# Performance work log

Hardware: AMD Instinct MI355X
Metric: run time of the kernel (lower is better)

The kernel has to match this reference:

```python
import jax, jax.numpy as jnp
import numpy as np

B, N, L, OUT = 64, 100, 32, 3
EDGE_SIZES = [64, 64]   # edge MLP widths per mp step
NODE_SIZES = [64, 32]   # node MLP widths per mp step
ALPHA = 0.1             # leaky relu slope
NUM_MPS = 2
EPS = 1e-12             # for differentiable euclidean norm


def _lin_init(key, fan_in, fan_out):
    k1, k2 = jax.random.split(key)
    s = 1.0 / np.sqrt(fan_in)
    w = jax.random.uniform(k1, (fan_in, fan_out), jnp.float32, -s, s)
    b = jax.random.uniform(k2, (fan_out,), jnp.float32, -s, s)
    return w, b


def setup_inputs() -> dict:
    key = jax.random.key(0)
    ks = iter(jax.random.split(key, 32))
    inp = {"x": jax.random.normal(next(ks), (B, L), jnp.float32)}
    # global latent map: Linear(L, N*L)
    inp["lin_w"], inp["lin_b"] = _lin_init(next(ks), L, N * L)
    d = L
    for i in range(NUM_MPS):
        e_in = 2 * d + 1  # [x_i, x_j, dist_ij]
        inp[f"e{i}_w0"], inp[f"e{i}_b0"] = _lin_init(next(ks), e_in, EDGE_SIZES[0])
        inp[f"e{i}_w1"], inp[f"e{i}_b1"] = _lin_init(next(ks), EDGE_SIZES[0], EDGE_SIZES[1])
        n_in = d + EDGE_SIZES[1]  # [x, aggregated edges]
        inp[f"n{i}_w0"], inp[f"n{i}_b0"] = _lin_init(next(ks), n_in, NODE_SIZES[0])
        inp[f"n{i}_w1"], inp[f"n{i}_b1"] = _lin_init(next(ks), NODE_SIZES[0], NODE_SIZES[1])
        d = NODE_SIZES[1]
    inp["out_w"], inp["out_b"] = _lin_init(next(ks), d, OUT)
    return inp


def _mlp(h, layers, alpha):
    for w, b in layers:
        h = jax.nn.leaky_relu(h @ w + b, alpha)
    return h


def _forward(x, lin_w, lin_b,
             e0_w0, e0_b0, e0_w1, e0_b1, n0_w0, n0_b0, n0_w1, n0_b1,
             e1_w0, e1_b0, e1_w1, e1_b1, n1_w0, n1_b0, n1_w1, n1_b1,
             out_w, out_b):
    # latent map: [B, L] -> [B, N, L]
    h = (x @ lin_w + lin_b).reshape(-1, N, L)
    steps = [
        ([(e0_w0, e0_b0), (e0_w1, e0_b1)], [(n0_w0, n0_b0), (n0_w1, n0_b1)]),
        ([(e1_w0, e1_b0), (e1_w1, e1_b1)], [(n1_w0, n1_b0), (n1_w1, n1_b1)]),
    ]
    for edge_layers, node_layers in steps:
        b, n, d = h.shape
        xi = h[:, :, None, :]  # [B, N, 1, d] (receiver)
        xj = h[:, None, :, :]  # [B, 1, N, d] (sender)
        # euclidean pairwise distance, eps for differentiability at 0
        dist = jnp.sqrt(jnp.sum((xi - xj) ** 2, axis=-1, keepdims=True) + EPS)
        e_in = jnp.concatenate([
            jnp.broadcast_to(xi, (b, n, n, d)),
            jnp.broadcast_to(xj, (b, n, n, d)),
            dist,
        ], axis=-1)                       # [B, N, N, 2d+1]
        A = _mlp(e_in, edge_layers, ALPHA)  # [B, N, N, e_out]
        agg = A.sum(axis=2)               # sum over senders -> [B, N, e_out]
        h = _mlp(jnp.concatenate([h, agg], axis=-1), node_layers, ALPHA)
    out = h @ out_w + out_b               # [B, N, OUT]
    return jnp.tanh(out)                  # normalize_output=True


def reference(x, lin_w, lin_b,
              e0_w0, e0_b0, e0_w1, e0_b1, n0_w0, n0_b0, n0_w1, n0_b1,
              e1_w0, e1_b0, e1_w1, e1_b1, n1_w0, n1_b0, n1_w1, n1_b1,
              out_w, out_b):
    return _forward(x, lin_w, lin_b,
                    e0_w0, e0_b0, e0_w1, e0_b1, n0_w0, n0_b0, n0_w1, n0_b1,
                    e1_w0, e1_b0, e1_w1, e1_b1, n1_w0, n1_b0, n1_w1, n1_b1,
                    out_w, out_b)
```

## Files before the change

kernel.cpp:

```cpp
#include <hip/hip_runtime.h>

#define NB 64
#define NN 100
#define DL 32
#define BN (NB * NN)

typedef _Float16 f16x8 __attribute__((ext_vector_type(8)));
typedef _Float16 f16x4 __attribute__((ext_vector_type(4)));
typedef float f32x4 __attribute__((ext_vector_type(4)));

static __device__ __forceinline__ float lrelu(float x) { return fmaxf(x, 0.1f * x); }

__global__ __launch_bounds__(256) void k_pre(
    const float* __restrict__ x, const float* __restrict__ lw, const float* __restrict__ lb,
    const float* __restrict__ ew0, const float* __restrict__ eb0,
    const float* __restrict__ w1a, const float* __restrict__ w1b,
    float* __restrict__ h, float* __restrict__ U, float* __restrict__ V,
    _Float16* __restrict__ PW) {
    int blk = blockIdx.x;
    int t = threadIdx.x;
    if (blk >= 1600) {
        int step = blk - 1600;
        const float* w1 = step ? w1b : w1a;
        _Float16* dst = PW + step * 4096;
#pragma unroll
        for (int u = 0; u < 16; ++u) {
            int idx = t * 16 + u;
            int jj = idx & 7, lane = (idx >> 3) & 63, hf = (idx >> 9) & 1, kt = idx >> 10;
            int c = hf * 32 + (lane >> 4) * 8 + jj;
            int k = kt * 16 + (lane & 15);
            dst[idx] = (_Float16)w1[c * 64 + k];
        }
        return;
    }
    __shared__ float xs[DL];
    __shared__ float hs[4][DL];
    int row0 = blk * 4;
    int b = row0 / NN;
    if (t < DL) xs[t] = x[b * DL + t];
    __syncthreads();
    if (t < 128) {
        int ni = t >> 5, c = t & 31;
        int n = (row0 + ni) % NN;
        float s = lb[n * DL + c];
#pragma unroll
        for (int cc = 0; cc < DL; ++cc) s += xs[cc] * lw[cc * 3200 + n * DL + c];
        hs[ni][c] = s;
        h[(row0 + ni) * DL + c] = s;
    }
    __syncthreads();
#pragma unroll
    for (int r = 0; r < 2; ++r) {
        int o = r * 256 + t;
        int ni = o >> 7, kw = o & 127;
        int which = kw >> 6, k = kw & 63;
        const float* wp = ew0 + (which ? DL * 64 : 0) + k;
        float s = which ? 0.f : eb0[k];
#pragma unroll
        for (int c = 0; c < DL; ++c) s += hs[ni][c] * wp[c * 64];
        (which ? V : U)[(row0 + ni) * 64 + k] = s;
    }
}

template <int FINAL>
__global__ __launch_bounds__(256) void k_edge_fused(
    const float* __restrict__ h, const float* __restrict__ U, const float* __restrict__ V,
    const float* __restrict__ w0, const _Float16* __restrict__ PW,
    const float* __restrict__ b1,
    const float* __restrict__ w0n, const float* __restrict__ b0n,
    const float* __restrict__ w1n, const float* __restrict__ b1n,
    const float* __restrict__ wA, const float* __restrict__ bA,
    float* __restrict__ hout, float* __restrict__ Uo, float* __restrict__ Vo,
    float* __restrict__ out) {
    __shared__ float dist[112];
    __shared__ _Float16 P[2][16][72];
    __shared__ float hs[DL];
    __shared__ float aggs[64];
    __shared__ float t0s[64];
    __shared__ float hs2[DL];
    __shared__ float red[4][64];

    int bi = blockIdx.x;
    int b = bi / NN;
    int t = threadIdx.x;
    int w = t >> 6, lane = t & 63, q = lane >> 4, kk = lane & 15;

    if (t < 112) {
        int j = t < NN ? t : NN - 1;
        const float* hi = h + bi * DL;
        const float* hj = h + (b * NN + j) * DL;
        float s = 0.f;
#pragma unroll
        for (int c = 0; c < DL; ++c) {
            float d = hi[c] - hj[c];
            s += d * d;
        }
        dist[t] = sqrtf(s + 1e-12f);
    }
    if (t < DL) hs[t] = h[bi * DL + t];

    int bj = t & 15, c0 = (t >> 4) * 4;
    float4 uvq = *(const float4*)(U + bi * 64 + c0);
    float4 wdq = *(const float4*)(w0 + 64 * 64 + c0);

    const f16x8* pw = (const f16x8*)PW;
    f16x8 Bf0 = pw[(w * 2 + 0) * 64 + lane];
    f16x8 Bf1 = pw[(w * 2 + 1) * 64 + lane];
    float b1k = b1[w * 16 + kk];
    f32x4 sacc = {0.f, 0.f, 0.f, 0.f};

    __syncthreads();

    {
        float dj = dist[bj];
        float4 v4 = *(const float4*)(V + (size_t)(b * NN + bj) * 64 + c0);
        f16x4 pv;
        pv[0] = (_Float16)lrelu(uvq.x + v4.x + dj * wdq.x);
        pv[1] = (_Float16)lrelu(uvq.y + v4.y + dj * wdq.y);
        pv[2] = (_Float16)lrelu(uvq.z + v4.z + dj * wdq.z);
        pv[3] = (_Float16)lrelu(uvq.w + v4.w + dj * wdq.w);
        *(f16x4*)&P[0][bj][c0] = pv;
    }
    __syncthreads();

#pragma unroll
    for (int jt = 0; jt < 7; ++jt) {
        f16x8 A0 = *(const f16x8*)&P[jt & 1][kk][q * 8];
        f16x8 A1 = *(const f16x8*)&P[jt & 1][kk][32 + q * 8];
        float4 vn;
        float djn = 0.f;
        if (jt < 6) {
            int j = (jt + 1) * 16 + bj;
            int jc = j < NN ? j : NN - 1;
            djn = dist[j];
            vn = *(const float4*)(V + (size_t)(b * NN + jc) * 64 + c0);
        }
        f32x4 a = {0.f, 0.f, 0.f, 0.f};
        a = __builtin_amdgcn_mfma_f32_16x16x32_f16(A0, Bf0, a, 0, 0, 0);
        a = __builtin_amdgcn_mfma_f32_16x16x32_f16(A1, Bf1, a, 0, 0, 0);
#pragma unroll
        for (int r = 0; r < 4; ++r) {
            int jr = jt * 16 + q * 4 + r;
            float v = lrelu(a[r] + b1k);
            sacc[r] += (jr < NN) ? v : 0.f;
        }
        if (jt < 6) {
            f16x4 pv;
            pv[0] = (_Float16)lrelu(uvq.x + vn.x + djn * wdq.x);
            pv[1] = (_Float16)lrelu(uvq.y + vn.y + djn * wdq.y);
            pv[2] = (_Float16)lrelu(uvq.z + vn.z + djn * wdq.z);
            pv[3] = (_Float16)lrelu(uvq.w + vn.w + djn * wdq.w);
            *(f16x4*)&P[(jt + 1) & 1][bj][c0] = pv;
        }
        __syncthreads();
    }

    {
        float s = sacc[0] + sacc[1] + sacc[2] + sacc[3];
        s += __shfl_xor(s, 16);
        s += __shfl_xor(s, 32);
        if (q == 0) aggs[w * 16 + kk] = s;
    }
    __syncthreads();

    {
        int k = t & 63, p = t >> 6;
        float s = 0.f;
#pragma unroll
        for (int ii = 0; ii < 24; ++ii) {
            int c = p * 24 + ii;
            float xv = (c < DL) ? hs[c] : aggs[c - DL];
            s += xv * w0n[c * 64 + k];
        }
        red[p][k] = s;
    }
    __syncthreads();
    if (t < 64) t0s[t] = lrelu(b0n[t] + red[0][t] + red[1][t] + red[2][t] + red[3][t]);
    __syncthreads();
    if (t < 64) {
        int k = t & 31, p = t >> 5;
        float s = 0.f;
#pragma unroll
        for (int ii = 0; ii < 32; ++ii) {
            int c = p * 32 + ii;
            s += t0s[c] * w1n[c * DL + k];
        }
        red[p][k] = s;
    }
    __syncthreads();
    if (t < DL) {
        float hv = lrelu(b1n[t] + red[0][t] + red[1][t]);
        hs2[t] = hv;
        if (!FINAL) hout[bi * DL + t] = hv;
    }
    __syncthreads();
    if (FINAL) {
        if (t < 3) {
            float s = bA[t];
#pragma unroll
            for (int c = 0; c < DL; ++c) s += hs2[c] * wA[c * 3 + t];
            out[bi * 3 + t] = tanhf(s);
        }
    } else if (t < 128) {
        int k = t & 63, which = t >> 6;
        const float* wp = wA + (which ? DL * 64 : 0) + k;
        float s = which ? 0.f : bA[k];
#pragma unroll
        for (int c = 0; c < DL; ++c) s += hs2[c] * wp[c * 64];
        (which ? Vo : Uo)[bi * 64 + k] = s;
    }
}

extern "C" void kernel_launch(void* const* d_in, const int* in_sizes, int n_in,
                              void* d_out, int out_size, void* d_ws, size_t ws_size,
                              hipStream_t stream) {
    const float* x     = (const float*)d_in[0];
    const float* lin_w = (const float*)d_in[1];
    const float* lin_b = (const float*)d_in[2];
    const float* ew0[2] = {(const float*)d_in[3],  (const float*)d_in[11]};
    const float* eb0[2] = {(const float*)d_in[4],  (const float*)d_in[12]};
    const float* ew1[2] = {(const float*)d_in[5],  (const float*)d_in[13]};
    const float* eb1[2] = {(const float*)d_in[6],  (const float*)d_in[14]};
    const float* nw0[2] = {(const float*)d_in[7],  (const float*)d_in[15]};
    const float* nb0[2] = {(const float*)d_in[8],  (const float*)d_in[16]};
    const float* nw1[2] = {(const float*)d_in[9],  (const float*)d_in[17]};
    const float* nb1[2] = {(const float*)d_in[10], (const float*)d_in[18]};
    const float* ow = (const float*)d_in[19];
    const float* ob = (const float*)d_in[20];
    float* out = (float*)d_out;

    float* h   = (float*)d_ws;
    float* h2  = h + 204800;
    float* U   = h2 + 204800;
    float* V   = U + 409600;
    float* U2  = V + 409600;
    float* V2  = U2 + 409600;
    _Float16* PW = (_Float16*)(V2 + 409600);

    k_pre<<<1602, 256, 0, stream>>>(x, lin_w, lin_b, ew0[0], eb0[0], ew1[0], ew1[1],
                                    h, U, V, PW);
    k_edge_fused<0><<<BN, 256, 0, stream>>>(h, U, V, ew0[0], PW, eb1[0],
                                            nw0[0], nb0[0], nw1[0], nb1[0],
                                            ew0[1], eb0[1], h2, U2, V2, nullptr);
    k_edge_fused<1><<<BN, 256, 0, stream>>>(h2, U2, V2, ew0[1], PW + 4096, eb1[1],
                                            nw0[1], nb0[1], nw1[1], nb1[1],
                                            ow, ob, nullptr, nullptr, nullptr, out);
}
```

Baseline: 189.4 us.

## Map one receiver node per wavefront and pre-transpose node MLP weights

The edge kernel now handles four receiver nodes per block, one per wavefront, instead of one node per 256-thread block. Each wave builds its MFMA A operands directly in registers, drops the per-tile shared-memory staging and block barriers, and covers all 64 output channels with four MFMA tiles. The edge weight fragments are staged once per block in LDS. The preprocessing kernel also transposes the node-MLP, next-step U/V and output weights so each lane can read contiguous vector rows. This trades more register pressure and more per-lane work in the node MLP for fewer barriers and fewer blocks.

```diff
diff --git a/kernel.cpp b/kernel.cpp
--- a/kernel.cpp
+++ b/kernel.cpp
@@ -6,30 +6,68 @@
 #define BN (NB * NN)
 
 typedef _Float16 f16x8 __attribute__((ext_vector_type(8)));
-typedef _Float16 f16x4 __attribute__((ext_vector_type(4)));
 typedef float f32x4 __attribute__((ext_vector_type(4)));
 
 static __device__ __forceinline__ float lrelu(float x) { return fmaxf(x, 0.1f * x); }
+static __device__ __forceinline__ f32x4 lrelu4(f32x4 x) {
+    return __builtin_elementwise_max(x, 0.1f * x);
+}
+static __device__ __forceinline__ f32x4 ld4(const float* p) { return *(const f32x4*)p; }
+static __device__ __forceinline__ float hsum4(f32x4 v) { return v[0] + v[1] + v[2] + v[3]; }
 
 __global__ __launch_bounds__(256) void k_pre(
     const float* __restrict__ x, const float* __restrict__ lw, const float* __restrict__ lb,
-    const float* __restrict__ ew0, const float* __restrict__ eb0,
+    const float* __restrict__ ew0a, const float* __restrict__ eb0a,
     const float* __restrict__ w1a, const float* __restrict__ w1b,
+    const float* __restrict__ nw0a, const float* __restrict__ nw0b,
+    const float* __restrict__ nw1a, const float* __restrict__ nw1b,
+    const float* __restrict__ ew0b, const float* __restrict__ ow,
     float* __restrict__ h, float* __restrict__ U, float* __restrict__ V,
-    _Float16* __restrict__ PW) {
+    _Float16* __restrict__ PW,
+    float* __restrict__ tw0n, float* __restrict__ tw1n,
+    float* __restrict__ tuv, float* __restrict__ owt) {
     int blk = blockIdx.x;
     int t = threadIdx.x;
     if (blk >= 1600) {
-        int step = blk - 1600;
-        const float* w1 = step ? w1b : w1a;
-        _Float16* dst = PW + step * 4096;
-#pragma unroll
-        for (int u = 0; u < 16; ++u) {
-            int idx = t * 16 + u;
-            int jj = idx & 7, lane = (idx >> 3) & 63, hf = (idx >> 9) & 1, kt = idx >> 10;
-            int c = hf * 32 + (lane >> 4) * 8 + jj;
-            int k = kt * 16 + (lane & 15);
-            dst[idx] = (_Float16)w1[c * 64 + k];
+        if (blk < 1602) {
+            int step = blk - 1600;
+            const float* w1 = step ? w1b : w1a;
+            _Float16* dst = PW + step * 4096;
+#pragma unroll
+            for (int u = 0; u < 16; ++u) {
+                int idx = t * 16 + u;
+                int jj = idx & 7, lane = (idx >> 3) & 63, hf = (idx >> 9) & 1, kt = idx >> 10;
+                int c = hf * 32 + (lane >> 4) * 8 + jj;
+                int k = kt * 16 + (lane & 15);
+                dst[idx] = (_Float16)w1[c * 64 + k];
+            }
+        } else if (blk < 1604) {
+            int s = blk - 1602;
+            const float* src = s ? nw0b : nw0a;
+            float* dst = tw0n + s * 6144;
+            for (int u = t; u < 6144; u += 256) {
+                int k = u / 96, c = u - k * 96;
+                dst[u] = src[c * 64 + k];
+            }
+        } else if (blk < 1606) {
+            int s = blk - 1604;
+            const float* src = s ? nw1b : nw1a;
+            float* dst = tw1n + s * 2048;
+            for (int u = t; u < 2048; u += 256) {
+                int k = u >> 6, c = u & 63;
+                dst[u] = src[c * 32 + k];
+            }
+        } else if (blk == 1606) {
+            for (int u = t; u < 4096; u += 256) {
+                int r = u >> 5, c = u & 31;
+                int k = r & 63, half = r >> 6;
+                tuv[u] = ew0b[(half * 32 + c) * 64 + k];
+            }
+        } else {
+            if (t < 96) {
+                int k = t >> 5, c = t & 31;
+                owt[t] = ow[c * 3 + k];
+            }
         }
         return;
     }
@@ -54,8 +92,8 @@
         int o = r * 256 + t;
         int ni = o >> 7, kw = o & 127;
         int which = kw >> 6, k = kw & 63;
-        const float* wp = ew0 + (which ? DL * 64 : 0) + k;
-        float s = which ? 0.f : eb0[k];
+        const float* wp = ew0a + (which ? DL * 64 : 0) + k;
+        float s = which ? 0.f : eb0a[k];
 #pragma unroll
         for (int c = 0; c < DL; ++c) s += hs[ni][c] * wp[c * 64];
         (which ? V : U)[(row0 + ni) * 64 + k] = s;
@@ -63,151 +101,169 @@
 }
 
 template <int FINAL>
-__global__ __launch_bounds__(256) void k_edge_fused(
+__global__ __launch_bounds__(256) void k_edge(
     const float* __restrict__ h, const float* __restrict__ U, const float* __restrict__ V,
     const float* __restrict__ w0, const _Float16* __restrict__ PW,
     const float* __restrict__ b1,
-    const float* __restrict__ w0n, const float* __restrict__ b0n,
-    const float* __restrict__ w1n, const float* __restrict__ b1n,
+    const float* __restrict__ tw0n, const float* __restrict__ b0n,
+    const float* __restrict__ tw1n, const float* __restrict__ b1n,
     const float* __restrict__ wA, const float* __restrict__ bA,
     float* __restrict__ hout, float* __restrict__ Uo, float* __restrict__ Vo,
     float* __restrict__ out) {
-    __shared__ float dist[112];
-    __shared__ _Float16 P[2][16][72];
-    __shared__ float hs[DL];
-    __shared__ float aggs[64];
-    __shared__ float t0s[64];
-    __shared__ float hs2[DL];
-    __shared__ float red[4][64];
-
-    int bi = blockIdx.x;
+    __shared__ __align__(16) _Float16 pwl[4096];
+    __shared__ float sdist[4][112];
+    __shared__ __align__(16) float sxin[4][96];
+    __shared__ __align__(16) float st0[4][64];
+    __shared__ __align__(16) float sh2[4][32];
+
+    int t = threadIdx.x;
+    {
+        const f16x8* srcp = (const f16x8*)PW;
+        f16x8* dstp = (f16x8*)pwl;
+        dstp[t] = srcp[t];
+        dstp[t + 256] = srcp[t + 256];
+    }
+    int w = t >> 6, lane = t & 63, q = lane >> 4, kk = lane & 15;
+    int bi = blockIdx.x * 4 + w;
     int b = bi / NN;
-    int t = threadIdx.x;
-    int w = t >> 6, lane = t & 63, q = lane >> 4, kk = lane & 15;
-
-    if (t < 112) {
-        int j = t < NN ? t : NN - 1;
-        const float* hi = h + bi * DL;
-        const float* hj = h + (b * NN + j) * DL;
-        float s = 0.f;
-#pragma unroll
-        for (int c = 0; c < DL; ++c) {
-            float d = hi[c] - hj[c];
-            s += d * d;
-        }
-        dist[t] = sqrtf(s + 1e-12f);
-    }
-    if (t < DL) hs[t] = h[bi * DL + t];
-
-    int bj = t & 15, c0 = (t >> 4) * 4;
-    float4 uvq = *(const float4*)(U + bi * 64 + c0);
-    float4 wdq = *(const float4*)(w0 + 64 * 64 + c0);
-
-    const f16x8* pw = (const f16x8*)PW;
-    f16x8 Bf0 = pw[(w * 2 + 0) * 64 + lane];
-    f16x8 Bf1 = pw[(w * 2 + 1) * 64 + lane];
-    float b1k = b1[w * 16 + kk];
-    f32x4 sacc = {0.f, 0.f, 0.f, 0.f};
+
+    if (lane < 32) sxin[w][lane] = h[bi * DL + lane];
+    const float* hb = h + b * NN * DL;
+    for (int jj = lane; jj < 112; jj += 64) {
+        int jc = jj < NN ? jj : NN - 1;
+        const float* hj = hb + jc * DL;
+        f32x4 s4 = {0.f, 0.f, 0.f, 0.f};
+#pragma unroll
+        for (int c4 = 0; c4 < 8; ++c4) {
+            f32x4 hi4 = ld4(&sxin[w][c4 * 4]);
+            f32x4 hj4 = ld4(&hj[c4 * 4]);
+            f32x4 d = hi4 - hj4;
+            s4 += d * d;
+        }
+        sdist[w][jj] = sqrtf(hsum4(s4) + 1e-12f);
+    }
+
+    int c0 = q * 8;
+    const float* Up = U + (size_t)bi * 64;
+    f32x4 u0 = ld4(Up + c0), u1 = ld4(Up + c0 + 4);
+    f32x4 u2 = ld4(Up + 32 + c0), u3 = ld4(Up + 36 + c0);
+    const float* wd = w0 + 64 * 64;
+    f32x4 d0 = ld4(wd + c0), d1 = ld4(wd + c0 + 4);
+    f32x4 d2 = ld4(wd + 32 + c0), d3 = ld4(wd + 36 + c0);
+    float b1k[4];
+#pragma unroll
+    for (int kt = 0; kt < 4; ++kt) b1k[kt] = b1[kt * 16 + kk];
+    float m6 = (q == 0) ? 1.f : 0.f;
 
     __syncthreads();
 
+    f32x4 sacc[4];
+    f32x4 zero4 = {0.f, 0.f, 0.f, 0.f};
+#pragma unroll
+    for (int kt = 0; kt < 4; ++kt) sacc[kt] = zero4;
+    const float* Vb = V + (size_t)b * NN * 64;
+
+    f32x4 v0, v1, v2, v3;
+    float dj;
     {
-        float dj = dist[bj];
-        float4 v4 = *(const float4*)(V + (size_t)(b * NN + bj) * 64 + c0);
-        f16x4 pv;
-        pv[0] = (_Float16)lrelu(uvq.x + v4.x + dj * wdq.x);
-        pv[1] = (_Float16)lrelu(uvq.y + v4.y + dj * wdq.y);
-        pv[2] = (_Float16)lrelu(uvq.z + v4.z + dj * wdq.z);
-        pv[3] = (_Float16)lrelu(uvq.w + v4.w + dj * wdq.w);
-        *(f16x4*)&P[0][bj][c0] = pv;
-    }
-    __syncthreads();
+        const float* vr = Vb + kk * 64 + c0;
+        v0 = ld4(vr); v1 = ld4(vr + 4); v2 = ld4(vr + 32); v3 = ld4(vr + 36);
+        dj = sdist[w][kk];
+    }
 
 #pragma unroll
     for (int jt = 0; jt < 7; ++jt) {
-        f16x8 A0 = *(const f16x8*)&P[jt & 1][kk][q * 8];
-        f16x8 A1 = *(const f16x8*)&P[jt & 1][kk][32 + q * 8];
-        float4 vn;
-        float djn = 0.f;
+        f32x4 cv0 = v0, cv1 = v1, cv2 = v2, cv3 = v3;
+        float cdj = dj;
         if (jt < 6) {
-            int j = (jt + 1) * 16 + bj;
-            int jc = j < NN ? j : NN - 1;
-            djn = dist[j];
-            vn = *(const float4*)(V + (size_t)(b * NN + jc) * 64 + c0);
-        }
-        f32x4 a = {0.f, 0.f, 0.f, 0.f};
-        a = __builtin_amdgcn_mfma_f32_16x16x32_f16(A0, Bf0, a, 0, 0, 0);
-        a = __builtin_amdgcn_mfma_f32_16x16x32_f16(A1, Bf1, a, 0, 0, 0);
-#pragma unroll
-        for (int r = 0; r < 4; ++r) {
-            int jr = jt * 16 + q * 4 + r;
-            float v = lrelu(a[r] + b1k);
-            sacc[r] += (jr < NN) ? v : 0.f;
-        }
-        if (jt < 6) {
-            f16x4 pv;
-            pv[0] = (_Float16)lrelu(uvq.x + vn.x + djn * wdq.x);
-            pv[1] = (_Float16)lrelu(uvq.y + vn.y + djn * wdq.y);
-            pv[2] = (_Float16)lrelu(uvq.z + vn.z + djn * wdq.z);
-            pv[3] = (_Float16)lrelu(uvq.w + vn.w + djn * wdq.w);
-            *(f16x4*)&P[(jt + 1) & 1][bj][c0] = pv;
-        }
-        __syncthreads();
-    }
-
-    {
-        float s = sacc[0] + sacc[1] + sacc[2] + sacc[3];
+            int j = (jt + 1) * 16 + kk;
+            int jc = (jt == 5 && j >= NN) ? NN - 1 : j;
+            const float* vr = Vb + jc * 64 + c0;
+            v0 = ld4(vr); v1 = ld4(vr + 4); v2 = ld4(vr + 32); v3 = ld4(vr + 36);
+            dj = sdist[w][j];
+        }
+        f32x4 p0 = lrelu4(u0 + cv0 + cdj * d0);
+        f32x4 p1 = lrelu4(u1 + cv1 + cdj * d1);
+        f32x4 p2 = lrelu4(u2 + cv2 + cdj * d2);
+        f32x4 p3 = lrelu4(u3 + cv3 + cdj * d3);
+        f16x8 A0, A1;
+        A0[0] = (_Float16)p0[0]; A0[1] = (_Float16)p0[1];
+        A0[2] = (_Float16)p0[2]; A0[3] = (_Float16)p0[3];
+        A0[4] = (_Float16)p1[0]; A0[5] = (_Float16)p1[1];
+        A0[6] = (_Float16)p1[2]; A0[7] = (_Float16)p1[3];
+        A1[0] = (_Float16)p2[0]; A1[1] = (_Float16)p2[1];
+        A1[2] = (_Float16)p2[2]; A1[3] = (_Float16)p2[3];
+        A1[4] = (_Float16)p3[0]; A1[5] = (_Float16)p3[1];
+        A1[6] = (_Float16)p3[2]; A1[7] = (_Float16)p3[3];
+#pragma unroll
+        for (int kt = 0; kt < 4; ++kt) {
+            f16x8 B0 = *(const f16x8*)&pwl[(kt * 2 + 0) * 512 + lane * 8];
+            f16x8 B1 = *(const f16x8*)&pwl[(kt * 2 + 1) * 512 + lane * 8];
+            f32x4 a = zero4;
+            a = __builtin_amdgcn_mfma_f32_16x16x32_f16(A0, B0, a, 0, 0, 0);
+            a = __builtin_amdgcn_mfma_f32_16x16x32_f16(A1, B1, a, 0, 0, 0);
+            f32x4 lr = lrelu4(a + b1k[kt]);
+            if (jt == 6) lr *= m6;
+            sacc[kt] += lr;
+        }
+    }
+
+    float ag[4];
+#pragma unroll
+    for (int kt = 0; kt < 4; ++kt) {
+        float s = hsum4(sacc[kt]);
         s += __shfl_xor(s, 16);
         s += __shfl_xor(s, 32);
-        if (q == 0) aggs[w * 16 + kk] = s;
-    }
-    __syncthreads();
+        ag[kt] = s;
+    }
+    if (lane < 16) {
+#pragma unroll
+        for (int kt = 0; kt < 4; ++kt) sxin[w][32 + kt * 16 + lane] = ag[kt];
+    }
 
     {
-        int k = t & 63, p = t >> 6;
-        float s = 0.f;
-#pragma unroll
-        for (int ii = 0; ii < 24; ++ii) {
-            int c = p * 24 + ii;
-            float xv = (c < DL) ? hs[c] : aggs[c - DL];
-            s += xv * w0n[c * 64 + k];
-        }
-        red[p][k] = s;
-    }
-    __syncthreads();
-    if (t < 64) t0s[t] = lrelu(b0n[t] + red[0][t] + red[1][t] + red[2][t] + red[3][t]);
-    __syncthreads();
-    if (t < 64) {
-        int k = t & 31, p = t >> 5;
-        float s = 0.f;
-#pragma unroll
-        for (int ii = 0; ii < 32; ++ii) {
-            int c = p * 32 + ii;
-            s += t0s[c] * w1n[c * DL + k];
-        }
-        red[p][k] = s;
-    }
-    __syncthreads();
-    if (t < DL) {
-        float hv = lrelu(b1n[t] + red[0][t] + red[1][t]);
-        hs2[t] = hv;
-        if (!FINAL) hout[bi * DL + t] = hv;
-    }
-    __syncthreads();
+        const float* wr = tw0n + lane * 96;
+        f32x4 acc = zero4;
+#pragma unroll
+        for (int cc = 0; cc < 24; ++cc) acc += ld4(&sxin[w][cc * 4]) * ld4(wr + cc * 4);
+        float s = hsum4(acc) + b0n[lane];
+        st0[w][lane] = lrelu(s);
+    }
+    {
+        int k2 = lane & 31, p = lane >> 5;
+        const float* wr = tw1n + k2 * 64 + p * 32;
+        f32x4 acc = zero4;
+#pragma unroll
+        for (int cc = 0; cc < 8; ++cc) acc += ld4(&st0[w][p * 32 + cc * 4]) * ld4(wr + cc * 4);
+        float s = hsum4(acc);
+        s += __shfl_xor(s, 32);
+        if (lane < 32) {
+            float hv = lrelu(s + b1n[lane]);
+            sh2[w][lane] = hv;
+            if (!FINAL) hout[bi * DL + lane] = hv;
+        }
+    }
+
     if (FINAL) {
-        if (t < 3) {
-            float s = bA[t];
-#pragma unroll
-            for (int c = 0; c < DL; ++c) s += hs2[c] * wA[c * 3 + t];
-            out[bi * 3 + t] = tanhf(s);
-        }
-    } else if (t < 128) {
-        int k = t & 63, which = t >> 6;
-        const float* wp = wA + (which ? DL * 64 : 0) + k;
-        float s = which ? 0.f : bA[k];
-#pragma unroll
-        for (int c = 0; c < DL; ++c) s += hs2[c] * wp[c * 64];
-        (which ? Vo : Uo)[bi * 64 + k] = s;
+        if (lane < 3) {
+            const float* wr = wA + lane * 32;
+            f32x4 acc = zero4;
+#pragma unroll
+            for (int cc = 0; cc < 8; ++cc) acc += ld4(&sh2[w][cc * 4]) * ld4(wr + cc * 4);
+            out[bi * 3 + lane] = tanhf(hsum4(acc) + bA[lane]);
+        }
+    } else {
+        const float* tu = wA + lane * 32;
+        const float* tv = wA + (64 + lane) * 32;
+        f32x4 au = zero4, av = zero4;
+#pragma unroll
+        for (int cc = 0; cc < 8; ++cc) {
+            f32x4 h4 = ld4(&sh2[w][cc * 4]);
+            au += h4 * ld4(tu + cc * 4);
+            av += h4 * ld4(tv + cc * 4);
+        }
+        Uo[bi * 64 + lane] = hsum4(au) + bA[lane];
+        Vo[bi * 64 + lane] = hsum4(av);
     }
 }
 
@@ -229,20 +285,25 @@
     const float* ob = (const float*)d_in[20];
     float* out = (float*)d_out;
 
-    float* h   = (float*)d_ws;
-    float* h2  = h + 204800;
-    float* U   = h2 + 204800;
-    float* V   = U + 409600;
-    float* U2  = V + 409600;
-    float* V2  = U2 + 409600;
+    float* h    = (float*)d_ws;
+    float* h2   = h + 204800;
+    float* U    = h2 + 204800;
+    float* V    = U + 409600;
+    float* U2   = V + 409600;
+    float* V2   = U2 + 409600;
     _Float16* PW = (_Float16*)(V2 + 409600);
-
-    k_pre<<<1602, 256, 0, stream>>>(x, lin_w, lin_b, ew0[0], eb0[0], ew1[0], ew1[1],
-                                    h, U, V, PW);
-    k_edge_fused<0><<<BN, 256, 0, stream>>>(h, U, V, ew0[0], PW, eb1[0],
-                                            nw0[0], nb0[0], nw1[0], nb1[0],
-                                            ew0[1], eb0[1], h2, U2, V2, nullptr);
-    k_edge_fused<1><<<BN, 256, 0, stream>>>(h2, U2, V2, ew0[1], PW + 4096, eb1[1],
-                                            nw0[1], nb0[1], nw1[1], nb1[1],
-                                            ow, ob, nullptr, nullptr, nullptr, out);
+    float* TW0n = (float*)(PW + 8192);
+    float* TW1n = TW0n + 12288;
+    float* TUV  = TW1n + 4096;
+    float* OWT  = TUV + 4096;
+
+    k_pre<<<1608, 256, 0, stream>>>(x, lin_w, lin_b, ew0[0], eb0[0], ew1[0], ew1[1],
+                                    nw0[0], nw0[1], nw1[0], nw1[1], ew0[1], ow,
+                                    h, U, V, PW, TW0n, TW1n, TUV, OWT);
+    k_edge<0><<<1600, 256, 0, stream>>>(h, U, V, ew0[0], PW, eb1[0],
+                                        TW0n, nb0[0], TW1n, nb1[0],
+                                        TUV, eb0[1], h2, U2, V2, nullptr);
+    k_edge<1><<<1600, 256, 0, stream>>>(h2, U2, V2, ew0[1], PW + 4096, eb1[1],
+                                        TW0n + 6144, nb0[1], TW1n + 2048, nb1[1],
+                                        OWT, ob, nullptr, nullptr, nullptr, out);
 }
```

After: 238.1 us. +25.8%, slower.
